# Kernel tuning notes

Measured on AMD Instinct MI355X. Metric: run time of the kernel, lower is better.

The kernel has to match this reference:

```python
import jax, jax.numpy as jnp
import numpy as np

B, S = 8, 512                  # batch, seq_len
V, H, L = 30522, 768, 12       # vocab, hidden, layers
NH, F, T, P = 12, 3072, 2, 512 # heads, ffn dim, type vocab, max positions
D = H // NH
EPS = 1e-12


def layer_norm(x, scale, bias):
    mu = jnp.mean(x, axis=-1, keepdims=True)
    var = jnp.mean((x - mu) ** 2, axis=-1, keepdims=True)
    return (x - mu) * jax.lax.rsqrt(var + EPS) * scale + bias


def setup_inputs() -> dict:
    key = jax.random.key(0)
    ks = jax.random.split(key, 16)
    p = lambda k, shp: (0.02 * jax.random.normal(k, shp, dtype=jnp.float32))
    return {
        "input_ids": jax.random.randint(ks[0], (B, S), 0, V, dtype=jnp.int32),
        "type_ids": jax.random.randint(ks[1], (B, S), 0, T, dtype=jnp.int32),
        "word_emb": p(ks[2], (V, H)),
        "pos_emb": p(ks[3], (P, H)),
        "type_emb": p(ks[4], (T, H)),
        "emb_ln_scale": jnp.ones((H,), jnp.float32),
        "emb_ln_bias": jnp.zeros((H,), jnp.float32),
        "wq": p(ks[5], (L, H, H)), "bq": jnp.zeros((L, H), jnp.float32),
        "wk": p(ks[6], (L, H, H)), "bk": jnp.zeros((L, H), jnp.float32),
        "wv": p(ks[7], (L, H, H)), "bv": jnp.zeros((L, H), jnp.float32),
        "wo": p(ks[8], (L, H, H)), "bo": jnp.zeros((L, H), jnp.float32),
        "ln1_scale": jnp.ones((L, H), jnp.float32), "ln1_bias": jnp.zeros((L, H), jnp.float32),
        "w1": p(ks[9], (L, H, F)), "b1": jnp.zeros((L, F), jnp.float32),
        "w2": p(ks[10], (L, F, H)), "b2": jnp.zeros((L, H), jnp.float32),
        "ln2_scale": jnp.ones((L, H), jnp.float32), "ln2_bias": jnp.zeros((L, H), jnp.float32),
    }


def reference(input_ids, type_ids, word_emb, pos_emb, type_emb, emb_ln_scale,
              emb_ln_bias, wq, bq, wk, bk, wv, bv, wo, bo, ln1_scale, ln1_bias,
              w1, b1, w2, b2, ln2_scale, ln2_bias):
    # padding mask: 1.0 where token id == 0, shape [B,1,1,S]
    mask = (input_ids == 0).astype(jnp.float32)[:, None, None, :]
    # embeddings: word + position + segment, then layernorm (dropout off / eval)
    h = word_emb[input_ids] + pos_emb[None, :S, :] + type_emb[type_ids]
    h = layer_norm(h, emb_ln_scale, emb_ln_bias)

    def block(x, lp):
        (wq_, bq_, wk_, bk_, wv_, bv_, wo_, bo_, l1s, l1b,
         w1_, b1_, w2_, b2_, l2s, l2b) = lp
        def heads(y, w, b):  # [B,S,H] -> [B,NH,S,D]
            return (y @ w + b).reshape(B, S, NH, D).transpose(0, 2, 1, 3)
        q = heads(x, wq_, bq_)
        k = heads(x, wk_, bk_)
        v = heads(x, wv_, bv_)
        logits = jnp.einsum('bhqd,bhkd->bhqk', q, k) / jnp.sqrt(jnp.float32(D))
        logits = logits + mask * -10000.0
        attn = jax.nn.softmax(logits, axis=-1)
        ctx = jnp.einsum('bhqk,bhkd->bhqd', attn, v)
        ctx = ctx.transpose(0, 2, 1, 3).reshape(B, S, H)
        x = layer_norm(x + ctx @ wo_ + bo_, l1s, l1b)
        ffn = jax.nn.gelu(x @ w1_ + b1_, approximate=False) @ w2_ + b2_
        x = layer_norm(x + ffn, l2s, l2b)
        return x, None

    h, _ = jax.lax.scan(block, h, (wq, bq, wk, bk, wv, bv, wo, bo,
                                   ln1_scale, ln1_bias, w1, b1, w2, b2,
                                   ln2_scale, ln2_bias))
    return h
```

## Files before the change

kernel.cpp:

```cpp
#include <hip/hip_runtime.h>
#include <hip/hip_bf16.h>
#include <math.h>

#define S_LEN   512
#define HID     768
#define NLAYER  12
#define NHEAD   12
#define FFN_DIM 3072
#define HDIM    64
#define NTOK    4096
#define QKVN    2304

typedef __bf16 bf16x8 __attribute__((ext_vector_type(8)));
typedef float  f32x4  __attribute__((ext_vector_type(4)));
typedef unsigned short us8 __attribute__((ext_vector_type(8)));

typedef __attribute__((address_space(1))) const unsigned int gas_u32;
typedef __attribute__((address_space(3))) unsigned int las_u32;

#define MFMA16(a, b, c) __builtin_amdgcn_mfma_f32_16x16x32_bf16((a), (b), (c), 0, 0, 0)

__device__ __forceinline__ void block_reduce_2(float& sum, float& sq) {
  __shared__ float sd[8];
  int lane = threadIdx.x & 63;
  int wid  = threadIdx.x >> 6;
  #pragma unroll
  for (int off = 32; off > 0; off >>= 1) {
    sum += __shfl_down(sum, off, 64);
    sq  += __shfl_down(sq,  off, 64);
  }
  if (lane == 0) { sd[wid] = sum; sd[4 + wid] = sq; }
  __syncthreads();
  sum = sd[0] + sd[1] + sd[2] + sd[3];
  sq  = sd[4] + sd[5] + sd[6] + sd[7];
}

__global__ __launch_bounds__(256) void mask_kernel(const int* __restrict__ ids,
                                                   float* __restrict__ mb) {
  int i = blockIdx.x * 256 + threadIdx.x;
  if (i < NTOK) mb[i] = (ids[i] == 0) ? -10000.0f : 0.0f;
}

__global__ __launch_bounds__(256) void pack_qkvb_kernel(
    const float* __restrict__ bq, const float* __restrict__ bk,
    const float* __restrict__ bv, float* __restrict__ out) {
  int i = blockIdx.x * 256 + threadIdx.x;
  if (i >= NLAYER * QKVN) return;
  int l = i / QKVN, c = i % QKVN;
  float v = (c < HID) ? bq[l * HID + c]
          : (c < 2 * HID) ? bk[l * HID + c - HID]
                          : bv[l * HID + c - 2 * HID];
  out[i] = v;
}

__global__ __launch_bounds__(256) void embed_ln_kernel(
    const int* __restrict__ ids, const int* __restrict__ tids,
    const float* __restrict__ we, const float* __restrict__ pe,
    const float* __restrict__ te, const float* __restrict__ gamma,
    const float* __restrict__ beta, float* __restrict__ out32,
    __bf16* __restrict__ out16) {
  int t = blockIdx.x;
  int s = t & (S_LEN - 1);
  int id = ids[t];
  int tp = tids[t];
  float x[3];
  #pragma unroll
  for (int i = 0; i < 3; ++i) {
    int c = threadIdx.x + i * 256;
    x[i] = we[(size_t)id * HID + c] + pe[(size_t)s * HID + c] +
           te[(size_t)tp * HID + c];
  }
  float sum = x[0] + x[1] + x[2];
  float sq  = x[0]*x[0] + x[1]*x[1] + x[2]*x[2];
  block_reduce_2(sum, sq);
  float mu   = sum * (1.0f / HID);
  float var  = sq * (1.0f / HID) - mu * mu;
  float rstd = rsqrtf(var + 1e-12f);
  #pragma unroll
  for (int i = 0; i < 3; ++i) {
    int c = threadIdx.x + i * 256;
    float v = (x[i] - mu) * rstd * gamma[c] + beta[c];
    out32[(size_t)t * HID + c] = v;
    out16[(size_t)t * HID + c] = (__bf16)v;
  }
}

__global__ __launch_bounds__(256) void add_ln_kernel(
    const float* __restrict__ a, const float* __restrict__ b,
    const float* __restrict__ gamma, const float* __restrict__ beta,
    float* __restrict__ out32, __bf16* __restrict__ out16) {
  int t = blockIdx.x;
  float x[3];
  #pragma unroll
  for (int i = 0; i < 3; ++i) {
    int c = threadIdx.x + i * 256;
    size_t idx = (size_t)t * HID + c;
    x[i] = a[idx] + b[idx];
  }
  float sum = x[0] + x[1] + x[2];
  float sq  = x[0]*x[0] + x[1]*x[1] + x[2]*x[2];
  block_reduce_2(sum, sq);
  float mu   = sum * (1.0f / HID);
  float var  = sq * (1.0f / HID) - mu * mu;
  float rstd = rsqrtf(var + 1e-12f);
  #pragma unroll
  for (int i = 0; i < 3; ++i) {
    int c = threadIdx.x + i * 256;
    float v = (x[i] - mu) * rstd * gamma[c] + beta[c];
    out32[(size_t)t * HID + c] = v;
    out16[(size_t)t * HID + c] = (__bf16)v;
  }
}

__global__ __launch_bounds__(256) void tcvt_kernel(
    const float* __restrict__ src, __bf16* __restrict__ dst, int R, int C) {
  __shared__ float tile[32][33];
  int c0 = blockIdx.x * 32, r0 = blockIdx.y * 32;
  int tx = threadIdx.x & 31, ty = threadIdx.x >> 5;
  #pragma unroll
  for (int i = 0; i < 4; ++i) {
    int r = ty + i * 8;
    tile[r][tx] = src[(size_t)(r0 + r) * C + c0 + tx];
  }
  __syncthreads();
  #pragma unroll
  for (int i = 0; i < 4; ++i) {
    int r = ty + i * 8;
    dst[(size_t)(c0 + r) * R + r0 + tx] = (__bf16)tile[tx][r];
  }
}

__global__ __launch_bounds__(256) void tcvt4_kernel(
    const float* __restrict__ s0, const float* __restrict__ s1,
    const float* __restrict__ s2, const float* __restrict__ s3,
    __bf16* __restrict__ d0, __bf16* __restrict__ d1,
    __bf16* __restrict__ d2, __bf16* __restrict__ d3) {
  __shared__ float tile[32][33];
  const float* src = (blockIdx.z == 0) ? s0 : (blockIdx.z == 1) ? s1
                   : (blockIdx.z == 2) ? s2 : s3;
  __bf16* dst = (blockIdx.z == 0) ? d0 : (blockIdx.z == 1) ? d1
              : (blockIdx.z == 2) ? d2 : d3;
  int c0 = blockIdx.x * 32, r0 = blockIdx.y * 32;
  int tx = threadIdx.x & 31, ty = threadIdx.x >> 5;
  #pragma unroll
  for (int i = 0; i < 4; ++i) {
    int r = ty + i * 8;
    tile[r][tx] = src[(size_t)(r0 + r) * HID + c0 + tx];
  }
  __syncthreads();
  #pragma unroll
  for (int i = 0; i < 4; ++i) {
    int r = ty + i * 8;
    dst[(size_t)(c0 + r) * HID + r0 + tx] = (__bf16)tile[tx][r];
  }
}

__global__ __launch_bounds__(256) void vtrans_kernel(
    const __bf16* __restrict__ qkv, __bf16* __restrict__ vt) {
  __shared__ __bf16 tile[32][33];
  int bh = blockIdx.z;
  int b = bh / NHEAD, h = bh % NHEAD;
  int s0 = blockIdx.x * 32, d0 = blockIdx.y * 32;
  int tx = threadIdx.x & 31, ty = threadIdx.x >> 5;
  #pragma unroll
  for (int i = 0; i < 4; ++i) {
    int r = ty + i * 8;
    tile[r][tx] = qkv[(size_t)(b * S_LEN + s0 + r) * QKVN + 2 * HID + h * HDIM + d0 + tx];
  }
  __syncthreads();
  #pragma unroll
  for (int i = 0; i < 4; ++i) {
    int r = ty + i * 8;
    vt[((size_t)bh * HDIM + d0 + r) * S_LEN + s0 + tx] = tile[tx][r];
  }
}

template <int MODE, int TN>
__global__ __launch_bounds__(256) void mfma_gemm(
    const __bf16* __restrict__ A, const __bf16* __restrict__ Bt,
    const float* __restrict__ bias, void* __restrict__ Cout,
    int M, int N, int K) {
  constexpr int AI = 4;
  constexpr int BI = TN / 32;
  constexpr int RT = (TN == 128) ? 4 : 2;
  constexpr int CT = 4;
  __shared__ __align__(16) __bf16 As[128 * 64];
  __shared__ __align__(16) __bf16 Bs[TN * 64];
  const int tid = threadIdx.x;
  const int w = tid >> 6, lane = tid & 63;
  const int l15 = lane & 15, quad = lane >> 4;
  const int m0 = blockIdx.y * 128, n0 = blockIdx.x * TN;
  const int lr = lane >> 3;
  const int colg = (lane & 7) ^ lr;

  const int wr = (TN == 128) ? (w >> 1) * 64 : w * 32;
  const int wc = (TN == 128) ? (w & 1) * 64 : 0;

  f32x4 acc[RT][CT];
  const f32x4 z4 = {0.f, 0.f, 0.f, 0.f};
  #pragma unroll
  for (int i = 0; i < RT; ++i)
    #pragma unroll
    for (int j = 0; j < CT; ++j) acc[i][j] = z4;

  const __bf16* Ag = A  + (size_t)(m0 + 8 * AI * w + lr) * K + colg * 8;
  const __bf16* Bg = Bt + (size_t)(n0 + 8 * BI * w + lr) * K + colg * 8;
  __bf16* Al = As + 512 * AI * w;
  __bf16* Bl = Bs + 512 * BI * w;

  for (int kt = 0; kt < K; kt += 64) {
    #pragma unroll
    for (int i = 0; i < AI; ++i)
      __builtin_amdgcn_global_load_lds(
          (gas_u32*)(Ag + (size_t)(8 * i) * K + kt),
          (las_u32*)(Al + 512 * i), 16, 0, 0);
    #pragma unroll
    for (int i = 0; i < BI; ++i)
      __builtin_amdgcn_global_load_lds(
          (gas_u32*)(Bg + (size_t)(8 * i) * K + kt),
          (las_u32*)(Bl + 512 * i), 16, 0, 0);
    __syncthreads();
    #pragma unroll
    for (int kc = 0; kc < 2; ++kc) {
      bf16x8 af[RT], bfr[CT];
      #pragma unroll
      for (int rt = 0; rt < RT; ++rt) {
        int row = wr + rt * 16 + l15;
        af[rt] = *(const bf16x8*)&As[(row * 8 + ((kc * 4 + quad) ^ (row & 7))) * 8];
      }
      #pragma unroll
      for (int ct = 0; ct < CT; ++ct) {
        int col = wc + ct * 16 + l15;
        bfr[ct] = *(const bf16x8*)&Bs[(col * 8 + ((kc * 4 + quad) ^ (col & 7))) * 8];
      }
      #pragma unroll
      for (int rt = 0; rt < RT; ++rt)
        #pragma unroll
        for (int ct = 0; ct < CT; ++ct)
          acc[rt][ct] = MFMA16(af[rt], bfr[ct], acc[rt][ct]);
    }
    __syncthreads();
  }

  #pragma unroll
  for (int rt = 0; rt < RT; ++rt) {
    int rbase = m0 + wr + rt * 16 + quad * 4;
    #pragma unroll
    for (int ct = 0; ct < CT; ++ct) {
      int col = n0 + wc + ct * 16 + l15;
      float bv = bias[col];
      #pragma unroll
      for (int r = 0; r < 4; ++r) {
        float v = acc[rt][ct][r] + bv;
        if (MODE == 2) v = 0.5f * v * (1.0f + erff(v * 0.70710678118654752f));
        if (MODE == 0)
          ((float*)Cout)[(size_t)(rbase + r) * N + col] = v;
        else
          ((__bf16*)Cout)[(size_t)(rbase + r) * N + col] = (__bf16)v;
      }
    }
  }
}

__global__ __launch_bounds__(256) void attn_mfma(
    const __bf16* __restrict__ qkv,
    const __bf16* __restrict__ vt,
    const float* __restrict__ mb,
    __bf16* __restrict__ ctx) {
  constexpr int PLD = 264;
  __shared__ __align__(16) __bf16 Plds[4][16 * PLD];
  const int tid = threadIdx.x;
  const int wv = tid >> 6, lane = tid & 63;
  const int l15 = lane & 15, quad = lane >> 4;
  const int b = blockIdx.z, hh = blockIdx.y, q0 = blockIdx.x * 64;
  const f32x4 z4 = {0.f, 0.f, 0.f, 0.f};

  size_t qoff = ((size_t)(b * S_LEN) + q0 + wv * 16 + l15) * QKVN + hh * HDIM;
  bf16x8 qa0 = *(const bf16x8*)(qkv + qoff + quad * 8);
  bf16x8 qa1 = *(const bf16x8*)(qkv + qoff + 32 + quad * 8);

  f32x4 sc[32];
  #pragma unroll
  for (int kt = 0; kt < 32; ++kt) {
    size_t koff = ((size_t)(b * S_LEN) + kt * 16 + l15) * QKVN + HID + hh * HDIM;
    bf16x8 kb0 = *(const bf16x8*)(qkv + koff + quad * 8);
    bf16x8 kb1 = *(const bf16x8*)(qkv + koff + 32 + quad * 8);
    f32x4 t = MFMA16(qa0, kb0, z4);
    sc[kt] = MFMA16(qa1, kb1, t);
  }

  float mx[4] = {-1e30f, -1e30f, -1e30f, -1e30f};
  #pragma unroll
  for (int kt = 0; kt < 32; ++kt) {
    float mval = mb[b * S_LEN + kt * 16 + l15];
    #pragma unroll
    for (int r = 0; r < 4; ++r) {
      float x = sc[kt][r] * 0.125f + mval;
      sc[kt][r] = x;
      mx[r] = fmaxf(mx[r], x);
    }
  }
  #pragma unroll
  for (int m = 1; m < 16; m <<= 1)
    #pragma unroll
    for (int r = 0; r < 4; ++r) mx[r] = fmaxf(mx[r], __shfl_xor(mx[r], m, 64));

  float sm[4] = {0.f, 0.f, 0.f, 0.f};
  #pragma unroll
  for (int kt = 0; kt < 32; ++kt)
    #pragma unroll
    for (int r = 0; r < 4; ++r) {
      float e = __expf(sc[kt][r] - mx[r]);
      sc[kt][r] = e;
      sm[r] += e;
    }
  #pragma unroll
  for (int m = 1; m < 16; m <<= 1)
    #pragma unroll
    for (int r = 0; r < 4; ++r) sm[r] += __shfl_xor(sm[r], m, 64);
  float inv[4];
  #pragma unroll
  for (int r = 0; r < 4; ++r) inv[r] = 1.0f / sm[r];

  __bf16* pbuf = &Plds[wv][0];
  const __bf16* vbase = vt + (size_t)(b * NHEAD + hh) * HDIM * S_LEN;
  f32x4 oc[4] = {z4, z4, z4, z4};
  #pragma unroll
  for (int half = 0; half < 2; ++half) {
    #pragma unroll
    for (int kt2 = 0; kt2 < 16; ++kt2) {
      int kt = half * 16 + kt2;
      #pragma unroll
      for (int r = 0; r < 4; ++r)
        pbuf[(quad * 4 + r) * PLD + kt2 * 16 + l15] = (__bf16)(sc[kt][r] * inv[r]);
    }
    #pragma unroll
    for (int kc = 0; kc < 8; ++kc) {
      bf16x8 pa = *(const bf16x8*)&pbuf[l15 * PLD + kc * 32 + quad * 8];
      int kbase = half * 256 + kc * 32;
      #pragma unroll
      for (int ct = 0; ct < 4; ++ct) {
        const __bf16* vp =
            vbase + (size_t)(ct * 16 + l15) * S_LEN + kbase + quad * 8;
        oc[ct] = MFMA16(pa, *(const bf16x8*)vp, oc[ct]);
      }
    }
  }

  int orow = b * S_LEN + q0 + wv * 16 + quad * 4;
  #pragma unroll
  for (int ct = 0; ct < 4; ++ct) {
    int col = hh * HDIM + ct * 16 + l15;
    #pragma unroll
    for (int r = 0; r < 4; ++r)
      ctx[(size_t)(orow + r) * HID + col] = (__bf16)oc[ct][r];
  }
}

extern "C" void kernel_launch(void* const* d_in, const int* in_sizes, int n_in,
                              void* d_out, int out_size, void* d_ws, size_t ws_size,
                              hipStream_t stream) {
  const int*   input_ids = (const int*)d_in[0];
  const int*   type_ids  = (const int*)d_in[1];
  const float* word_emb  = (const float*)d_in[2];
  const float* pos_emb   = (const float*)d_in[3];
  const float* type_emb  = (const float*)d_in[4];
  const float* eln_s     = (const float*)d_in[5];
  const float* eln_b     = (const float*)d_in[6];
  const float* wq = (const float*)d_in[7];
  const float* bq = (const float*)d_in[8];
  const float* wk = (const float*)d_in[9];
  const float* bk = (const float*)d_in[10];
  const float* wv = (const float*)d_in[11];
  const float* bv = (const float*)d_in[12];
  const float* wo = (const float*)d_in[13];
  const float* bo = (const float*)d_in[14];
  const float* l1s = (const float*)d_in[15];
  const float* l1b = (const float*)d_in[16];
  const float* w1  = (const float*)d_in[17];
  const float* b1  = (const float*)d_in[18];
  const float* w2  = (const float*)d_in[19];
  const float* b2  = (const float*)d_in[20];
  const float* l2s = (const float*)d_in[21];
  const float* l2b = (const float*)d_in[22];

  char* p = (char*)d_ws;
  float*   h32    = (float*)p;            p += (size_t)NTOK * HID * 4;
  float*   tmp32  = (float*)p;            p += (size_t)NTOK * HID * 4;
  __bf16*  vT16   = (__bf16*)tmp32;
  __bf16*  h16    = (__bf16*)p;           p += (size_t)NTOK * HID * 2;
  __bf16*  qkv16  = (__bf16*)p;           p += (size_t)NTOK * QKVN * 2;
  __bf16*  ctx16  = (__bf16*)p;           p += (size_t)NTOK * HID * 2;
  __bf16*  ffn16  = qkv16;
  __bf16*  wT     = (__bf16*)p;           p += (size_t)QKVN * HID * 2;
  __bf16*  woT    = (__bf16*)p;           p += (size_t)HID * HID * 2;
  __bf16*  w1T    = (__bf16*)p;           p += (size_t)HID * FFN_DIM * 2;
  __bf16*  w2T    = (__bf16*)p;           p += (size_t)HID * FFN_DIM * 2;
  float*   qkvb12 = (float*)p;            p += (size_t)NLAYER * QKVN * 4;
  float*   mb     = (float*)p;            p += (size_t)NTOK * 4;

  dim3 blk(256);
  mask_kernel<<<dim3(NTOK / 256), blk, 0, stream>>>(input_ids, mb);
  pack_qkvb_kernel<<<dim3((NLAYER * QKVN + 255) / 256), blk, 0, stream>>>(
      bq, bk, bv, qkvb12);
  embed_ln_kernel<<<dim3(NTOK), blk, 0, stream>>>(
      input_ids, type_ids, word_emb, pos_emb, type_emb, eln_s, eln_b, h32, h16);

  dim3 g_qkv(QKVN / 128, NTOK / 128);
  dim3 g_ff1(FFN_DIM / 128, NTOK / 128);
  dim3 g_h64(HID / 64, NTOK / 128);
  dim3 g_at(S_LEN / 64, NHEAD, 8);
  dim3 g_t4(HID / 32, HID / 32, 4);
  dim3 g_t2(FFN_DIM / 32, HID / 32);
  dim3 g_t3(HID / 32, FFN_DIM / 32);
  dim3 g_vt(S_LEN / 32, HDIM / 32, 8 * NHEAD);

  const size_t WHH = (size_t)HID * HID;
  const size_t WHF = (size_t)HID * FFN_DIM;

  for (int l = 0; l < NLAYER; ++l) {
    size_t boff = (size_t)l * HID;
    tcvt4_kernel<<<g_t4, blk, 0, stream>>>(
        wq + l * WHH, wk + l * WHH, wv + l * WHH, wo + l * WHH,
        wT, wT + WHH, wT + 2 * WHH, woT);
    tcvt_kernel<<<g_t2, blk, 0, stream>>>(w1 + l * WHF, w1T, HID, FFN_DIM);
    tcvt_kernel<<<g_t3, blk, 0, stream>>>(w2 + l * WHF, w2T, FFN_DIM, HID);

    mfma_gemm<1, 128><<<g_qkv, blk, 0, stream>>>(
        h16, wT, qkvb12 + (size_t)l * QKVN, qkv16, NTOK, QKVN, HID);
    vtrans_kernel<<<g_vt, blk, 0, stream>>>(qkv16, vT16);
    attn_mfma<<<g_at, blk, 0, stream>>>(qkv16, vT16, mb, ctx16);
    mfma_gemm<0, 64><<<g_h64, blk, 0, stream>>>(
        ctx16, woT, bo + boff, tmp32, NTOK, HID, HID);
    add_ln_kernel<<<dim3(NTOK), blk, 0, stream>>>(
        h32, tmp32, l1s + boff, l1b + boff, h32, h16);
    mfma_gemm<2, 128><<<g_ff1, blk, 0, stream>>>(
        h16, w1T, b1 + (size_t)l * FFN_DIM, ffn16, NTOK, FFN_DIM, HID);
    mfma_gemm<0, 64><<<g_h64, blk, 0, stream>>>(
        ffn16, w2T, b2 + boff, tmp32, NTOK, HID, FFN_DIM);
    float* dst = (l == NLAYER - 1) ? (float*)d_out : h32;
    add_ln_kernel<<<dim3(NTOK), blk, 0, stream>>>(
        h32, tmp32, l2s + boff, l2b + boff, dst, h16);
  }
}
```

Before: 2.853 ms.

## Batch weight transposes, fuse V-transpose into QKV GEMM, split-K FFN2, fast GELU

Converts all layers' weights to transposed bf16 in three upfront launches when the workspace allows, instead of per-layer conversions. Folds the V transpose into the QKV GEMM epilogue, which writes V straight into the transposed layout and removes vtrans_kernel. The second FFN GEMM gets a 2-way split-K whose partials are summed inside add_ln to raise block count. The erf-based GELU is replaced by a polynomial erf approximation, trading a little accuracy for fewer instructions.

```diff
diff --git a/kernel.cpp b/kernel.cpp
--- a/kernel.cpp
+++ b/kernel.cpp
@@ -12,13 +12,24 @@
 #define QKVN    2304
 
 typedef __bf16 bf16x8 __attribute__((ext_vector_type(8)));
+typedef __bf16 bf16x4 __attribute__((ext_vector_type(4)));
 typedef float  f32x4  __attribute__((ext_vector_type(4)));
-typedef unsigned short us8 __attribute__((ext_vector_type(8)));
 
 typedef __attribute__((address_space(1))) const unsigned int gas_u32;
 typedef __attribute__((address_space(3))) unsigned int las_u32;
 
 #define MFMA16(a, b, c) __builtin_amdgcn_mfma_f32_16x16x32_bf16((a), (b), (c), 0, 0, 0)
+
+__device__ __forceinline__ float fast_gelu(float v) {
+  float ax = fabsf(v) * 0.70710678118654752f;
+  float t  = __builtin_amdgcn_rcpf(fmaf(0.3275911f, ax, 1.0f));
+  float p  = fmaf(fmaf(fmaf(fmaf(1.061405429f, t, -1.453152027f), t,
+                            1.421413741f), t, -0.284496736f), t, 0.254829592f);
+  float e  = __expf(-ax * ax);
+  float er = 1.0f - p * t * e;
+  er = copysignf(er, v);
+  return 0.5f * v * (1.0f + er);
+}
 
 __device__ __forceinline__ void block_reduce_2(float& sum, float& sq) {
   __shared__ float sd[8];
@@ -87,15 +98,17 @@
 
 __global__ __launch_bounds__(256) void add_ln_kernel(
     const float* __restrict__ a, const float* __restrict__ b,
+    const float* __restrict__ c,
     const float* __restrict__ gamma, const float* __restrict__ beta,
     float* __restrict__ out32, __bf16* __restrict__ out16) {
   int t = blockIdx.x;
   float x[3];
   #pragma unroll
   for (int i = 0; i < 3; ++i) {
-    int c = threadIdx.x + i * 256;
-    size_t idx = (size_t)t * HID + c;
+    int ci = threadIdx.x + i * 256;
+    size_t idx = (size_t)t * HID + ci;
     x[i] = a[idx] + b[idx];
+    if (c) x[i] += c[idx];
   }
   float sum = x[0] + x[1] + x[2];
   float sq  = x[0]*x[0] + x[1]*x[1] + x[2]*x[2];
@@ -105,16 +118,19 @@
   float rstd = rsqrtf(var + 1e-12f);
   #pragma unroll
   for (int i = 0; i < 3; ++i) {
-    int c = threadIdx.x + i * 256;
-    float v = (x[i] - mu) * rstd * gamma[c] + beta[c];
-    out32[(size_t)t * HID + c] = v;
-    out16[(size_t)t * HID + c] = (__bf16)v;
+    int ci = threadIdx.x + i * 256;
+    float v = (x[i] - mu) * rstd * gamma[ci] + beta[ci];
+    out32[(size_t)t * HID + ci] = v;
+    out16[(size_t)t * HID + ci] = (__bf16)v;
   }
 }
 
 __global__ __launch_bounds__(256) void tcvt_kernel(
     const float* __restrict__ src, __bf16* __restrict__ dst, int R, int C) {
   __shared__ float tile[32][33];
+  int l = blockIdx.z;
+  src += (size_t)l * R * C;
+  dst += (size_t)l * R * C;
   int c0 = blockIdx.x * 32, r0 = blockIdx.y * 32;
   int tx = threadIdx.x & 31, ty = threadIdx.x >> 5;
   #pragma unroll
@@ -131,15 +147,17 @@
 }
 
 __global__ __launch_bounds__(256) void tcvt4_kernel(
-    const float* __restrict__ s0, const float* __restrict__ s1,
-    const float* __restrict__ s2, const float* __restrict__ s3,
-    __bf16* __restrict__ d0, __bf16* __restrict__ d1,
-    __bf16* __restrict__ d2, __bf16* __restrict__ d3) {
+    const float* __restrict__ sq, const float* __restrict__ sk,
+    const float* __restrict__ sv, const float* __restrict__ so,
+    __bf16* __restrict__ dqkv, __bf16* __restrict__ dwo) {
   __shared__ float tile[32][33];
-  const float* src = (blockIdx.z == 0) ? s0 : (blockIdx.z == 1) ? s1
-                   : (blockIdx.z == 2) ? s2 : s3;
-  __bf16* dst = (blockIdx.z == 0) ? d0 : (blockIdx.z == 1) ? d1
-              : (blockIdx.z == 2) ? d2 : d3;
+  const size_t WHH = (size_t)HID * HID;
+  int z = blockIdx.z;
+  int l = z >> 2, sel = z & 3;
+  const float* src = ((sel == 0) ? sq : (sel == 1) ? sk : (sel == 2) ? sv : so)
+                     + (size_t)l * WHH;
+  __bf16* dst = (sel < 3) ? dqkv + (size_t)l * 3 * WHH + (size_t)sel * WHH
+                          : dwo + (size_t)l * WHH;
   int c0 = blockIdx.x * 32, r0 = blockIdx.y * 32;
   int tx = threadIdx.x & 31, ty = threadIdx.x >> 5;
   #pragma unroll
@@ -152,26 +170,6 @@
   for (int i = 0; i < 4; ++i) {
     int r = ty + i * 8;
     dst[(size_t)(c0 + r) * HID + r0 + tx] = (__bf16)tile[tx][r];
-  }
-}
-
-__global__ __launch_bounds__(256) void vtrans_kernel(
-    const __bf16* __restrict__ qkv, __bf16* __restrict__ vt) {
-  __shared__ __bf16 tile[32][33];
-  int bh = blockIdx.z;
-  int b = bh / NHEAD, h = bh % NHEAD;
-  int s0 = blockIdx.x * 32, d0 = blockIdx.y * 32;
-  int tx = threadIdx.x & 31, ty = threadIdx.x >> 5;
-  #pragma unroll
-  for (int i = 0; i < 4; ++i) {
-    int r = ty + i * 8;
-    tile[r][tx] = qkv[(size_t)(b * S_LEN + s0 + r) * QKVN + 2 * HID + h * HDIM + d0 + tx];
-  }
-  __syncthreads();
-  #pragma unroll
-  for (int i = 0; i < 4; ++i) {
-    int r = ty + i * 8;
-    vt[((size_t)bh * HDIM + d0 + r) * S_LEN + s0 + tx] = tile[tx][r];
   }
 }
 
@@ -179,7 +177,7 @@
 __global__ __launch_bounds__(256) void mfma_gemm(
     const __bf16* __restrict__ A, const __bf16* __restrict__ Bt,
     const float* __restrict__ bias, void* __restrict__ Cout,
-    int M, int N, int K) {
+    __bf16* __restrict__ vtout, int M, int N, int K, int kchunk) {
   constexpr int AI = 4;
   constexpr int BI = TN / 32;
   constexpr int RT = (TN == 128) ? 4 : 2;
@@ -190,11 +188,15 @@
   const int w = tid >> 6, lane = tid & 63;
   const int l15 = lane & 15, quad = lane >> 4;
   const int m0 = blockIdx.y * 128, n0 = blockIdx.x * TN;
+  const int kz = blockIdx.z;
   const int lr = lane >> 3;
   const int colg = (lane & 7) ^ lr;
 
   const int wr = (TN == 128) ? (w >> 1) * 64 : w * 32;
   const int wc = (TN == 128) ? (w & 1) * 64 : 0;
+
+  A  += (size_t)kz * kchunk;
+  Bt += (size_t)kz * kchunk;
 
   f32x4 acc[RT][CT];
   const f32x4 z4 = {0.f, 0.f, 0.f, 0.f};
@@ -208,7 +210,7 @@
   __bf16* Al = As + 512 * AI * w;
   __bf16* Bl = Bs + 512 * BI * w;
 
-  for (int kt = 0; kt < K; kt += 64) {
+  for (int kt = 0; kt < kchunk; kt += 64) {
     #pragma unroll
     for (int i = 0; i < AI; ++i)
       __builtin_amdgcn_global_load_lds(
@@ -242,21 +244,36 @@
     __syncthreads();
   }
 
+  float* outf = (float*)Cout + (size_t)kz * M * N;
   #pragma unroll
   for (int rt = 0; rt < RT; ++rt) {
     int rbase = m0 + wr + rt * 16 + quad * 4;
     #pragma unroll
     for (int ct = 0; ct < CT; ++ct) {
       int col = n0 + wc + ct * 16 + l15;
-      float bv = bias[col];
+      float bv = (kz == 0) ? bias[col] : 0.0f;
+      float vv[4];
       #pragma unroll
       for (int r = 0; r < 4; ++r) {
         float v = acc[rt][ct][r] + bv;
-        if (MODE == 2) v = 0.5f * v * (1.0f + erff(v * 0.70710678118654752f));
-        if (MODE == 0)
-          ((float*)Cout)[(size_t)(rbase + r) * N + col] = v;
-        else
-          ((__bf16*)Cout)[(size_t)(rbase + r) * N + col] = (__bf16)v;
+        if (MODE == 2) v = fast_gelu(v);
+        vv[r] = v;
+      }
+      if (MODE == 3 && col >= 2 * HID) {
+        int cc = col - 2 * HID;
+        int hh = cc >> 6, d = cc & 63;
+        int bb = rbase >> 9, s0 = rbase & (S_LEN - 1);
+        bf16x4 pk = {(__bf16)vv[0], (__bf16)vv[1], (__bf16)vv[2], (__bf16)vv[3]};
+        *(bf16x4*)(vtout +
+                   (((size_t)(bb * NHEAD + hh) * HDIM + d) * S_LEN + s0)) = pk;
+      } else {
+        #pragma unroll
+        for (int r = 0; r < 4; ++r) {
+          if (MODE == 0)
+            outf[(size_t)(rbase + r) * N + col] = vv[r];
+          else
+            ((__bf16*)Cout)[(size_t)(rbase + r) * N + col] = (__bf16)vv[r];
+        }
       }
     }
   }
@@ -386,18 +403,30 @@
 
   char* p = (char*)d_ws;
   float*   h32    = (float*)p;            p += (size_t)NTOK * HID * 4;
-  float*   tmp32  = (float*)p;            p += (size_t)NTOK * HID * 4;
+  float*   tmp32  = (float*)p;            p += (size_t)NTOK * HID * 4 * 2;
+  float*   tmp32b = tmp32 + (size_t)NTOK * HID;
   __bf16*  vT16   = (__bf16*)tmp32;
   __bf16*  h16    = (__bf16*)p;           p += (size_t)NTOK * HID * 2;
   __bf16*  qkv16  = (__bf16*)p;           p += (size_t)NTOK * QKVN * 2;
   __bf16*  ctx16  = (__bf16*)p;           p += (size_t)NTOK * HID * 2;
   __bf16*  ffn16  = qkv16;
-  __bf16*  wT     = (__bf16*)p;           p += (size_t)QKVN * HID * 2;
-  __bf16*  woT    = (__bf16*)p;           p += (size_t)HID * HID * 2;
-  __bf16*  w1T    = (__bf16*)p;           p += (size_t)HID * FFN_DIM * 2;
-  __bf16*  w2T    = (__bf16*)p;           p += (size_t)HID * FFN_DIM * 2;
   float*   qkvb12 = (float*)p;            p += (size_t)NLAYER * QKVN * 4;
   float*   mb     = (float*)p;            p += (size_t)NTOK * 4;
+
+  const size_t WHH = (size_t)HID * HID;
+  const size_t WHF = (size_t)HID * FFN_DIM;
+  const size_t WQKV = (size_t)QKVN * HID;
+
+  size_t used = (size_t)(p - (char*)d_ws);
+  size_t needB = used + (WQKV + WHH + 2 * WHF) * 2 * NLAYER + 256;
+  int batched = (ws_size >= needB) ? 1 : 0;
+  int nl = batched ? NLAYER : 1;
+  __bf16* wTall  = (__bf16*)p;  p += WQKV * 2 * nl;
+  __bf16* woTall = (__bf16*)p;  p += WHH * 2 * nl;
+  __bf16* w1Tall = (__bf16*)p;  p += WHF * 2 * nl;
+  __bf16* w2Tall = (__bf16*)p;  p += WHF * 2 * nl;
+  size_t sQKV = batched ? WQKV : 0, sHH = batched ? WHH : 0,
+         sHF = batched ? WHF : 0;
 
   dim3 blk(256);
   mask_kernel<<<dim3(NTOK / 256), blk, 0, stream>>>(input_ids, mb);
@@ -406,40 +435,53 @@
   embed_ln_kernel<<<dim3(NTOK), blk, 0, stream>>>(
       input_ids, type_ids, word_emb, pos_emb, type_emb, eln_s, eln_b, h32, h16);
 
-  dim3 g_qkv(QKVN / 128, NTOK / 128);
-  dim3 g_ff1(FFN_DIM / 128, NTOK / 128);
-  dim3 g_h64(HID / 64, NTOK / 128);
+  if (batched) {
+    tcvt4_kernel<<<dim3(HID / 32, HID / 32, 4 * NLAYER), blk, 0, stream>>>(
+        wq, wk, wv, wo, wTall, woTall);
+    tcvt_kernel<<<dim3(FFN_DIM / 32, HID / 32, NLAYER), blk, 0, stream>>>(
+        w1, w1Tall, HID, FFN_DIM);
+    tcvt_kernel<<<dim3(HID / 32, FFN_DIM / 32, NLAYER), blk, 0, stream>>>(
+        w2, w2Tall, FFN_DIM, HID);
+  }
+
+  dim3 g_qkv(QKVN / 128, NTOK / 128, 1);
+  dim3 g_ff1(FFN_DIM / 128, NTOK / 128, 1);
+  dim3 g_wo(HID / 64, NTOK / 128, 1);
+  dim3 g_ff2(HID / 64, NTOK / 128, 2);
   dim3 g_at(S_LEN / 64, NHEAD, 8);
-  dim3 g_t4(HID / 32, HID / 32, 4);
-  dim3 g_t2(FFN_DIM / 32, HID / 32);
-  dim3 g_t3(HID / 32, FFN_DIM / 32);
-  dim3 g_vt(S_LEN / 32, HDIM / 32, 8 * NHEAD);
-
-  const size_t WHH = (size_t)HID * HID;
-  const size_t WHF = (size_t)HID * FFN_DIM;
 
   for (int l = 0; l < NLAYER; ++l) {
     size_t boff = (size_t)l * HID;
-    tcvt4_kernel<<<g_t4, blk, 0, stream>>>(
-        wq + l * WHH, wk + l * WHH, wv + l * WHH, wo + l * WHH,
-        wT, wT + WHH, wT + 2 * WHH, woT);
-    tcvt_kernel<<<g_t2, blk, 0, stream>>>(w1 + l * WHF, w1T, HID, FFN_DIM);
-    tcvt_kernel<<<g_t3, blk, 0, stream>>>(w2 + l * WHF, w2T, FFN_DIM, HID);
-
-    mfma_gemm<1, 128><<<g_qkv, blk, 0, stream>>>(
-        h16, wT, qkvb12 + (size_t)l * QKVN, qkv16, NTOK, QKVN, HID);
-    vtrans_kernel<<<g_vt, blk, 0, stream>>>(qkv16, vT16);
+    if (!batched) {
+      tcvt4_kernel<<<dim3(HID / 32, HID / 32, 4), blk, 0, stream>>>(
+          wq + l * WHH, wk + l * WHH, wv + l * WHH, wo + l * WHH,
+          wTall, woTall);
+      tcvt_kernel<<<dim3(FFN_DIM / 32, HID / 32, 1), blk, 0, stream>>>(
+          w1 + l * WHF, w1Tall, HID, FFN_DIM);
+      tcvt_kernel<<<dim3(HID / 32, FFN_DIM / 32, 1), blk, 0, stream>>>(
+          w2 + l * WHF, w2Tall, FFN_DIM, HID);
+    }
+    const __bf16* wTl  = wTall  + (size_t)l * sQKV;
+    const __bf16* woTl = woTall + (size_t)l * sHH;
+    const __bf16* w1Tl = w1Tall + (size_t)l * sHF;
+    const __bf16* w2Tl = w2Tall + (size_t)l * sHF;
+
+    mfma_gemm<3, 128><<<g_qkv, blk, 0, stream>>>(
+        h16, wTl, qkvb12 + (size_t)l * QKVN, qkv16, vT16,
+        NTOK, QKVN, HID, HID);
     attn_mfma<<<g_at, blk, 0, stream>>>(qkv16, vT16, mb, ctx16);
-    mfma_gemm<0, 64><<<g_h64, blk, 0, stream>>>(
-        ctx16, woT, bo + boff, tmp32, NTOK, HID, HID);
+    mfma_gemm<0, 64><<<g_wo, blk, 0, stream>>>(
+        ctx16, woTl, bo + boff, tmp32, nullptr, NTOK, HID, HID, HID);
     add_ln_kernel<<<dim3(NTOK), blk, 0, stream>>>(
-        h32, tmp32, l1s + boff, l1b + boff, h32, h16);
+        h32, tmp32, nullptr, l1s + boff, l1b + boff, h32, h16);
     mfma_gemm<2, 128><<<g_ff1, blk, 0, stream>>>(
-        h16, w1T, b1 + (size_t)l * FFN_DIM, ffn16, NTOK, FFN_DIM, HID);
-    mfma_gemm<0, 64><<<g_h64, blk, 0, stream>>>(
-        ffn16, w2T, b2 + boff, tmp32, NTOK, HID, FFN_DIM);
+        h16, w1Tl, b1 + (size_t)l * FFN_DIM, ffn16, nullptr,
+        NTOK, FFN_DIM, HID, HID);
+    mfma_gemm<0, 64><<<g_ff2, blk, 0, stream>>>(
+        ffn16, w2Tl, b2 + boff, tmp32, nullptr, NTOK, HID, FFN_DIM,
+        FFN_DIM / 2);
     float* dst = (l == NLAYER - 1) ? (float*)d_out : h32;
     add_ln_kernel<<<dim3(NTOK), blk, 0, stream>>>(
-        h32, tmp32, l2s + boff, l2b + boff, dst, h16);
-  }
-}
+        h32, tmp32, tmp32b, l2s + boff, l2b + boff, dst, h16);
+  }
+}
```

New measurement: 2.699 ms. 5.4% less time.
